# Kernel optimization log

Hardware: AMD Instinct MI355X
Metric: run time of the kernel (lower is better)

The kernel has to match this reference:

```python
import jax, jax.numpy as jnp
import numpy as np

N_NODES = 100000
N_EDGES = 1600000
IN_DIM = 192   # n_shapes(64) * n_dims(3)
H1, H2 = 64, 32


def _glorot(key, shape):
    lim = np.sqrt(6.0 / (shape[0] + shape[1])).astype(np.float32)
    return jax.random.uniform(key, shape, jnp.float32, -lim, lim)


def setup_inputs() -> dict:
    key = jax.random.key(0)
    ks = jax.random.split(key, 8)
    verts = jax.random.normal(ks[0], (N_NODES, IN_DIM), jnp.float32)
    edges = jax.random.randint(ks[1], (N_EDGES, 2), 0, N_NODES)
    return {
        "verts": verts,
        "edges": edges,
        "W0_1": _glorot(ks[2], (IN_DIM, H1)),
        "W1_1": _glorot(ks[3], (IN_DIM, H1)),
        "b1": jnp.zeros((H1,), jnp.float32),
        "W0_2": _glorot(ks[4], (H1, H2)),
        "W1_2": _glorot(ks[5], (H1, H2)),
        "b2": jnp.zeros((H2,), jnp.float32),
    }


def cheb_conv(x, src, dst, W0, W1, b, n):
    # ChebConv K=2 with lambda_max=2: L_hat = -D^{-1/2} A D^{-1/2} (zero diagonal)
    deg = jax.ops.segment_sum(jnp.ones(src.shape, x.dtype), src, num_segments=n)
    d_inv = jnp.where(deg > 0, jax.lax.rsqrt(jnp.maximum(deg, 1.0)), 0.0)
    norm = -d_inv[src] * d_inv[dst]                      # [E]
    Tx1 = jax.ops.segment_sum(norm[:, None] * x[src], dst, num_segments=n)  # [n,F]
    return x @ W0 + Tx1 @ W1 + b


def reference(verts, edges, W0_1, W1_1, b1, W0_2, W1_2, b2):
    n = verts.shape[0]
    src, dst = edges[:, 0], edges[:, 1]  # edge_index rows after edges.t()
    x = jax.nn.relu(cheb_conv(verts, src, dst, W0_1, W1_1, b1, n))
    return cheb_conv(x, src, dst, W0_2, W1_2, b2, n)
```

## Files before the change

kernel.cpp:

```cpp
#include <hip/hip_runtime.h>

#define N_NODES 100000
#define N_EDGES 1600000
#define IN_DIM  192
#define H1      64
#define H2      32
#define NBKT    391
#define CAP_D   4608
#define NP1     196
#define K1GRID  1759

typedef __attribute__((ext_vector_type(8))) short short8;
typedef __attribute__((ext_vector_type(4))) float f32x4;

__device__ inline short f2bf(float f) {
    union { float f; unsigned u; } v; v.f = f;
    unsigned r = (v.u + 0x7FFFu + ((v.u >> 16) & 1u)) >> 16;
    return (short)r;
}
__device__ inline float bf2f(unsigned short s) {
    union { unsigned u; float f; } v; v.u = ((unsigned)s) << 16;
    return v.f;
}

__global__ __launch_bounds__(256) void prep_w_kernel(
    const float* __restrict__ W0_1, const float* __restrict__ W1_1,
    const float* __restrict__ W0_2, const float* __restrict__ W1_2,
    short* __restrict__ Bt1, short* __restrict__ Bt2, int* __restrict__ bucket_next) {
    if (blockIdx.x == 0) {
        for (int i = threadIdx.x; i < 1024; i += 256)
            bucket_next[i] = (i & 511) * CAP_D;
    }
    int idx = blockIdx.x * 256 + threadIdx.x;
    if (idx < 128 * IN_DIM) {
        int n = idx / IN_DIM, k = idx % IN_DIM;
        float v = (n < H1) ? W0_1[(size_t)k * H1 + n] : W1_1[(size_t)k * H1 + (n - H1)];
        Bt1[idx] = f2bf(v);
    } else {
        int j = idx - 128 * IN_DIM;
        if (j < 64 * H1) {
            int n = j / H1, k = j % H1;
            float v = (n < H2) ? W0_2[(size_t)k * H2 + n] : W1_2[(size_t)k * H2 + (n - H2)];
            Bt2[j] = f2bf(v);
        }
    }
}

__global__ __launch_bounds__(256) void k1_fused(
    const int* __restrict__ edges, int* __restrict__ bucket_next,
    int* __restrict__ bins_dst, unsigned char* __restrict__ bins_src,
    const float* __restrict__ verts, const short* __restrict__ Bt1,
    const float* __restrict__ b1, short* __restrict__ hbase, short* __restrict__ y1b) {
    __shared__ int cntd[512];
    __shared__ int curd[512];
    __shared__ int cnts[512];
    __shared__ int curs[512];
    int b = blockIdx.x;
    int tid = threadIdx.x;
    if (b % 9 == 0) {
        int p = b / 9;
        cntd[tid] = 0; cntd[tid + 256] = 0;
        cnts[tid] = 0; cnts[tid + 256] = 0;
        __syncthreads();
        const int2* e2 = (const int2*)edges;
        int base = p * 8192;
        for (int c = 0; c < 4; ++c) {
            int ebase = base + c * 2048 + tid * 8;
#pragma unroll
            for (int i = 0; i < 8; ++i) {
                int e = ebase + i;
                if (e < N_EDGES) {
                    int2 ed = e2[e];
                    atomicAdd(&cntd[ed.y >> 8], 1);
                    atomicAdd(&cnts[ed.x >> 8], 1);
                }
            }
        }
        __syncthreads();
        {
            int c;
            c = cntd[tid];       curd[tid]       = (c > 0) ? atomicAdd(&bucket_next[tid], c) : 0;
            c = cntd[tid + 256]; curd[tid + 256] = (c > 0) ? atomicAdd(&bucket_next[tid + 256], c) : 0;
            c = cnts[tid];       curs[tid]       = (c > 0) ? atomicAdd(&bucket_next[512 + tid], c) : 0;
            c = cnts[tid + 256]; curs[tid + 256] = (c > 0) ? atomicAdd(&bucket_next[512 + tid + 256], c) : 0;
        }
        __syncthreads();
        for (int c = 0; c < 4; ++c) {
            int ebase = base + c * 2048 + tid * 8;
#pragma unroll
            for (int i = 0; i < 8; ++i) {
                int e = ebase + i;
                if (e < N_EDGES) {
                    int2 ed = e2[e];
                    int bd = ed.y >> 8;
                    int sd = atomicAdd(&curd[bd], 1);
                    if (sd < (bd + 1) * CAP_D)
                        bins_dst[sd] = ((ed.y & 255) << 17) | ed.x;
                    int bs = ed.x >> 8;
                    int ss = atomicAdd(&curs[bs], 1);
                    if (ss < (bs + 1) * CAP_D)
                        bins_src[ss] = (unsigned char)(ed.x & 255);
                }
            }
        }
        return;
    }
    int g = b - b / 9 - 1;
    int lane = tid & 63;
    int wave = tid >> 6;
    int rowbase = g * 64 + wave * 16;
    int lr = lane & 15;
    int lk = (lane >> 4) * 8;

    int row = rowbase + lr;
    int rc = (row < N_NODES) ? row : (N_NODES - 1);
    const float* p = verts + (size_t)rc * IN_DIM + lk;
    short8 a[6];
#pragma unroll
    for (int ks = 0; ks < 6; ++ks) {
        f32x4 u0 = *(const f32x4*)(p + ks * 32);
        f32x4 u1 = *(const f32x4*)(p + ks * 32 + 4);
        short8 t;
        t[0] = f2bf(u0[0]); t[1] = f2bf(u0[1]); t[2] = f2bf(u0[2]); t[3] = f2bf(u0[3]);
        t[4] = f2bf(u1[0]); t[5] = f2bf(u1[1]); t[6] = f2bf(u1[2]); t[7] = f2bf(u1[3]);
        a[ks] = t;
    }

    f32x4 acc[8] = {};
#pragma unroll
    for (int cf = 0; cf < 8; ++cf) {
        const short* bp = Bt1 + (size_t)(cf * 16 + lr) * IN_DIM + lk;
#pragma unroll
        for (int ks = 0; ks < 6; ++ks) {
            short8 bb = *(const short8*)(bp + ks * 32);
            acc[cf] = __builtin_amdgcn_mfma_f32_16x16x32_bf16(a[ks], bb, acc[cf], 0, 0, 0);
        }
    }

    int srow = (lane >> 4) * 4;
#pragma unroll
    for (int cf = 0; cf < 8; ++cf) {
        int colc = cf * 16 + lr;
        float bias = (colc < H1) ? b1[colc] : 0.f;
#pragma unroll
        for (int r = 0; r < 4; ++r) {
            int orow = rowbase + srow + r;
            if (orow < N_NODES) {
                float v = acc[cf][r];
                if (colc < H1) hbase[(size_t)orow * H1 + colc] = f2bf(v + bias);
                else           y1b[(size_t)orow * H1 + (colc - H1)] = f2bf(v);
            }
        }
    }
}

__global__ __launch_bounds__(256) void csr_kernel(
    const int* __restrict__ bins_dst, const unsigned char* __restrict__ bins_src,
    const int* __restrict__ bucket_next, float* __restrict__ dinv,
    int* __restrict__ row_beg, int* __restrict__ row_end, int* __restrict__ col,
    const unsigned short* __restrict__ y1b, short* __restrict__ y1s) {
    __shared__ int cnt_l[256];
    __shared__ int seg_l[256];
    __shared__ int s[256];
    __shared__ int dcnt[256];
    __shared__ float dinv_l[256];
    int b = blockIdx.x;
    int tid = threadIdx.x;
    int beg = b * CAP_D;
    int filld = bucket_next[b] - beg;
    if (filld > CAP_D) filld = CAP_D;
    int fills = bucket_next[512 + b] - beg;
    if (fills > CAP_D) fills = CAP_D;
    cnt_l[tid] = 0;
    dcnt[tid] = 0;
    __syncthreads();
    for (int i = tid; i < filld; i += 256)
        atomicAdd(&cnt_l[bins_dst[beg + i] >> 17], 1);
    for (int i = tid; i < fills; i += 256)
        atomicAdd(&dcnt[bins_src[beg + i]], 1);
    __syncthreads();
    int v = cnt_l[tid];
    s[tid] = v;
    __syncthreads();
    for (int off = 1; off < 256; off <<= 1) {
        int t = (tid >= off) ? s[tid - off] : 0;
        __syncthreads();
        s[tid] += t;
        __syncthreads();
    }
    int excl = s[tid] - v;
    seg_l[tid] = beg + excl;
    int n = b * 256 + tid;
    int d = dcnt[tid];
    float dv = (d > 0) ? rsqrtf((float)d) : 0.f;
    dinv_l[tid] = dv;
    if (n < N_NODES) {
        row_beg[n] = beg + excl;
        row_end[n] = beg + excl + v;
        dinv[n] = dv;
    }
    __syncthreads();
    for (int i = tid; i < filld; i += 256) {
        int w = bins_dst[beg + i];
        int slot = atomicAdd(&seg_l[w >> 17], 1);
        col[slot] = w & 0x1FFFF;
    }
    int nb = b * 256;
    int nmax = N_NODES - nb; if (nmax > 256) nmax = 256;
    for (int idx = tid; idx < nmax * 8; idx += 256) {
        int r = idx >> 3, j = idx & 7;
        float w = dinv_l[r];
        size_t off = (size_t)(nb + r) * H1 + j * 8;
        short8 vv = *(const short8*)&y1b[off];
        short8 o;
#pragma unroll
        for (int q = 0; q < 8; ++q) o[q] = f2bf(w * bf2f((unsigned short)vv[q]));
        *(short8*)&y1s[off] = o;
    }
}

__global__ __launch_bounds__(256) void g1g2_kernel(
    const int* __restrict__ row_beg, const int* __restrict__ row_end,
    const int* __restrict__ col, const float* __restrict__ dinv,
    const unsigned short* __restrict__ hbase, const unsigned short* __restrict__ y1s,
    const short* __restrict__ Bt2, const float* __restrict__ b2,
    float* __restrict__ out, short* __restrict__ y2s) {
    __shared__ short hb_l[16][68];
    int tid = threadIdx.x, lane = tid & 63, wv = tid >> 6;
    int nb = blockIdx.x * 16;
    for (int j = 0; j < 4; ++j) {
        int n = nb + wv * 4 + j;
        int beg = row_beg[n], end = row_end[n];
        float acc = 0.f;
        int i = beg;
        for (; i + 8 <= end; i += 8) {
            int s0 = col[i], s1 = col[i + 1], s2 = col[i + 2], s3 = col[i + 3];
            int s4 = col[i + 4], s5 = col[i + 5], s6 = col[i + 6], s7 = col[i + 7];
            float v0 = bf2f(y1s[(size_t)s0 * H1 + lane]);
            float v1 = bf2f(y1s[(size_t)s1 * H1 + lane]);
            float v2 = bf2f(y1s[(size_t)s2 * H1 + lane]);
            float v3 = bf2f(y1s[(size_t)s3 * H1 + lane]);
            float v4 = bf2f(y1s[(size_t)s4 * H1 + lane]);
            float v5 = bf2f(y1s[(size_t)s5 * H1 + lane]);
            float v6 = bf2f(y1s[(size_t)s6 * H1 + lane]);
            float v7 = bf2f(y1s[(size_t)s7 * H1 + lane]);
            acc += ((v0 + v1) + (v2 + v3)) + ((v4 + v5) + (v6 + v7));
        }
        for (; i + 4 <= end; i += 4) {
            int s0 = col[i], s1 = col[i + 1], s2 = col[i + 2], s3 = col[i + 3];
            float v0 = bf2f(y1s[(size_t)s0 * H1 + lane]);
            float v1 = bf2f(y1s[(size_t)s1 * H1 + lane]);
            float v2 = bf2f(y1s[(size_t)s2 * H1 + lane]);
            float v3 = bf2f(y1s[(size_t)s3 * H1 + lane]);
            acc += (v0 + v1) + (v2 + v3);
        }
        for (; i < end; ++i)
            acc += bf2f(y1s[(size_t)col[i] * H1 + lane]);
        float hf = bf2f(hbase[(size_t)n * H1 + lane]) - dinv[n] * acc;
        hb_l[wv * 4 + j][lane] = f2bf(fmaxf(hf, 0.f));
    }
    __syncthreads();
    int lr = lane & 15;
    int lk = (lane >> 4) * 8;
    short8 a0 = *(const short8*)&hb_l[lr][lk];
    short8 a1 = *(const short8*)&hb_l[lr][32 + lk];
    const short* bp = Bt2 + (size_t)(wv * 16 + lr) * H1 + lk;
    short8 b0 = *(const short8*)(bp);
    short8 b1 = *(const short8*)(bp + 32);
    f32x4 acc2 = {};
    acc2 = __builtin_amdgcn_mfma_f32_16x16x32_bf16(a0, b0, acc2, 0, 0, 0);
    acc2 = __builtin_amdgcn_mfma_f32_16x16x32_bf16(a1, b1, acc2, 0, 0, 0);
    int srow = (lane >> 4) * 4;
    int colc = wv * 16 + lr;
    float bias = (colc < H2) ? b2[colc] : 0.f;
#pragma unroll
    for (int r = 0; r < 4; ++r) {
        int n = nb + srow + r;
        float v = acc2[r];
        if (colc < H2) out[(size_t)n * H2 + colc] = v + bias;
        else           y2s[(size_t)n * H2 + (colc - H2)] = f2bf(dinv[n] * v);
    }
}

__global__ __launch_bounds__(256) void gather2_kernel(
    const int* __restrict__ row_beg, const int* __restrict__ row_end,
    const int* __restrict__ col, const float* __restrict__ dinv,
    const unsigned short* __restrict__ y2s, float* __restrict__ out) {
    int wave = (blockIdx.x * 256 + threadIdx.x) >> 6;
    int lane = threadIdx.x & 63;
    int n = wave * 2 + (lane >> 5);
    if (n >= N_NODES) return;
    int c32 = lane & 31;
    int beg = row_beg[n], end = row_end[n];
    float acc = 0.f;
    int i = beg;
    for (; i + 8 <= end; i += 8) {
        int s0 = col[i], s1 = col[i + 1], s2 = col[i + 2], s3 = col[i + 3];
        int s4 = col[i + 4], s5 = col[i + 5], s6 = col[i + 6], s7 = col[i + 7];
        float v0 = bf2f(y2s[(size_t)s0 * H2 + c32]);
        float v1 = bf2f(y2s[(size_t)s1 * H2 + c32]);
        float v2 = bf2f(y2s[(size_t)s2 * H2 + c32]);
        float v3 = bf2f(y2s[(size_t)s3 * H2 + c32]);
        float v4 = bf2f(y2s[(size_t)s4 * H2 + c32]);
        float v5 = bf2f(y2s[(size_t)s5 * H2 + c32]);
        float v6 = bf2f(y2s[(size_t)s6 * H2 + c32]);
        float v7 = bf2f(y2s[(size_t)s7 * H2 + c32]);
        acc += ((v0 + v1) + (v2 + v3)) + ((v4 + v5) + (v6 + v7));
    }
    for (; i + 4 <= end; i += 4) {
        int s0 = col[i], s1 = col[i + 1], s2 = col[i + 2], s3 = col[i + 3];
        float v0 = bf2f(y2s[(size_t)s0 * H2 + c32]);
        float v1 = bf2f(y2s[(size_t)s1 * H2 + c32]);
        float v2 = bf2f(y2s[(size_t)s2 * H2 + c32]);
        float v3 = bf2f(y2s[(size_t)s3 * H2 + c32]);
        acc += (v0 + v1) + (v2 + v3);
    }
    for (; i < end; ++i)
        acc += bf2f(y2s[(size_t)col[i] * H2 + c32]);
    size_t idx = (size_t)n * H2 + c32;
    out[idx] = out[idx] - dinv[n] * acc;
}

extern "C" void kernel_launch(void* const* d_in, const int* in_sizes, int n_in,
                              void* d_out, int out_size, void* d_ws, size_t ws_size,
                              hipStream_t stream) {
    const float* verts = (const float*)d_in[0];
    const int*   edges = (const int*)  d_in[1];
    const float* W0_1  = (const float*)d_in[2];
    const float* W1_1  = (const float*)d_in[3];
    const float* b1    = (const float*)d_in[4];
    const float* W0_2  = (const float*)d_in[5];
    const float* W1_2  = (const float*)d_in[6];
    const float* b2    = (const float*)d_in[7];
    float* out = (float*)d_out;

    char* ws = (char*)d_ws;
    auto align256 = [](size_t x) { return (x + 255) & ~(size_t)255; };
    size_t o = 0;
    auto alloc = [&](size_t bytes) { size_t r = o; o = align256(o + bytes); return r; };

    int*   bucket_next = (int*)  (ws + alloc((size_t)1024 * 4));
    int*   bins_dst    = (int*)  (ws + alloc((size_t)NBKT * CAP_D * 4));
    unsigned char* bins_src = (unsigned char*)(ws + alloc((size_t)NBKT * CAP_D));
    int*   col         = (int*)  (ws + alloc((size_t)NBKT * CAP_D * 4));
    int*   row_beg     = (int*)  (ws + alloc((size_t)N_NODES * 4));
    int*   row_end     = (int*)  (ws + alloc((size_t)N_NODES * 4));
    float* dinv        = (float*)(ws + alloc((size_t)N_NODES * 4));
    short* Bt1         = (short*)(ws + alloc((size_t)128 * IN_DIM * 2));
    short* Bt2         = (short*)(ws + alloc((size_t)64 * H1 * 2));
    short* hbase       = (short*)(ws + alloc((size_t)N_NODES * H1 * 2));
    short* y1b         = (short*)(ws + alloc((size_t)N_NODES * H1 * 2));
    short* y1s         = (short*)(ws + alloc((size_t)N_NODES * H1 * 2));
    short* y2s         = (short*)(ws + alloc((size_t)N_NODES * H2 * 2));

    prep_w_kernel<<<112, 256, 0, stream>>>(W0_1, W1_1, W0_2, W1_2, Bt1, Bt2, bucket_next);

    k1_fused  <<<K1GRID, 256, 0, stream>>>(edges, bucket_next, bins_dst, bins_src,
                                           verts, Bt1, b1, hbase, y1b);
    csr_kernel<<<NBKT, 256, 0, stream>>>(bins_dst, bins_src, bucket_next, dinv,
                                         row_beg, row_end, col,
                                         (const unsigned short*)y1b, y1s);

    g1g2_kernel<<<N_NODES / 16, 256, 0, stream>>>(row_beg, row_end, col, dinv,
                                                  (const unsigned short*)hbase,
                                                  (const unsigned short*)y1s,
                                                  Bt2, b2, out, y2s);
    gather2_kernel<<<(N_NODES + 7) / 8, 256, 0, stream>>>(row_beg, row_end, col, dinv,
                                                          (const unsigned short*)y2s, out);
}
```

Baseline: 210.3 us.

## Split edge binning into smaller blocks and keep edges in registers between passes

Each edge-binning block now handles 2048 edges instead of 8192, and one in every three blocks does binning instead of one in nine, giving 782 binning blocks alongside the same 1563 GEMM blocks. Each thread keeps its 8 edges in registers between the counting pass and the scatter pass, so edges are not read from global memory twice. This spreads the binning work over more blocks and removes the second edge read. In exchange it issues about four times as many global atomics on bucket_next, and more register state per thread could lower occupancy.

```diff
diff --git a/kernel.cpp b/kernel.cpp
--- a/kernel.cpp
+++ b/kernel.cpp
@@ -7,8 +7,7 @@
 #define H2      32
 #define NBKT    391
 #define CAP_D   4608
-#define NP1     196
-#define K1GRID  1759
+#define K1GRID  2345
 
 typedef __attribute__((ext_vector_type(8))) short short8;
 typedef __attribute__((ext_vector_type(4))) float f32x4;
@@ -57,24 +56,23 @@
     __shared__ int curs[512];
     int b = blockIdx.x;
     int tid = threadIdx.x;
-    if (b % 9 == 0) {
-        int p = b / 9;
+    if (b % 3 == 0) {
+        int p = b / 3;
         cntd[tid] = 0; cntd[tid + 256] = 0;
         cnts[tid] = 0; cnts[tid + 256] = 0;
         __syncthreads();
-        const int2* e2 = (const int2*)edges;
-        int base = p * 8192;
-        for (int c = 0; c < 4; ++c) {
-            int ebase = base + c * 2048 + tid * 8;
-#pragma unroll
-            for (int i = 0; i < 8; ++i) {
-                int e = ebase + i;
-                if (e < N_EDGES) {
-                    int2 ed = e2[e];
-                    atomicAdd(&cntd[ed.y >> 8], 1);
-                    atomicAdd(&cnts[ed.x >> 8], 1);
-                }
-            }
+        int ebase = p * 2048 + tid * 8;
+        int2 ed[8]; int bd[8], bs[8];
+#pragma unroll
+        for (int i = 0; i < 8; ++i) {
+            int e = ebase + i;
+            if (e < N_EDGES) {
+                ed[i] = ((const int2*)edges)[e];
+                bd[i] = ed[i].y >> 8;
+                bs[i] = ed[i].x >> 8;
+                atomicAdd(&cntd[bd[i]], 1);
+                atomicAdd(&cnts[bs[i]], 1);
+            } else { bd[i] = -1; bs[i] = -1; }
         }
         __syncthreads();
         {
@@ -85,27 +83,20 @@
             c = cnts[tid + 256]; curs[tid + 256] = (c > 0) ? atomicAdd(&bucket_next[512 + tid + 256], c) : 0;
         }
         __syncthreads();
-        for (int c = 0; c < 4; ++c) {
-            int ebase = base + c * 2048 + tid * 8;
-#pragma unroll
-            for (int i = 0; i < 8; ++i) {
-                int e = ebase + i;
-                if (e < N_EDGES) {
-                    int2 ed = e2[e];
-                    int bd = ed.y >> 8;
-                    int sd = atomicAdd(&curd[bd], 1);
-                    if (sd < (bd + 1) * CAP_D)
-                        bins_dst[sd] = ((ed.y & 255) << 17) | ed.x;
-                    int bs = ed.x >> 8;
-                    int ss = atomicAdd(&curs[bs], 1);
-                    if (ss < (bs + 1) * CAP_D)
-                        bins_src[ss] = (unsigned char)(ed.x & 255);
-                }
+#pragma unroll
+        for (int i = 0; i < 8; ++i) {
+            if (bd[i] >= 0) {
+                int sd = atomicAdd(&curd[bd[i]], 1);
+                if (sd < (bd[i] + 1) * CAP_D)
+                    bins_dst[sd] = ((ed[i].y & 255) << 17) | ed[i].x;
+                int ss = atomicAdd(&curs[bs[i]], 1);
+                if (ss < (bs[i] + 1) * CAP_D)
+                    bins_src[ss] = (unsigned char)(ed[i].x & 255);
             }
         }
         return;
     }
-    int g = b - b / 9 - 1;
+    int g = b - b / 3 - 1;
     int lane = tid & 63;
     int wave = tid >> 6;
     int rowbase = g * 64 + wave * 16;
```

New measurement: 197.6 us. 1.06x faster.
